# Kernel optimization log

Measured on AMD Instinct MI355X. Metric: run time of the kernel, lower is better.

## Reference

```python
import jax, jax.numpy as jnp
import numpy as np

NY, NU, NH = 64, 64, 256  # Nhidden=256 -> 128 complex eigen pairs
T, NB = 4096, 32          # horizon, batch


def setup_inputs() -> dict:
    key = jax.random.key(0)
    ks = jax.random.split(key, 9)
    return {
        "y0": jax.random.normal(ks[0], (NB, NY), jnp.float32),
        "U": jax.random.normal(ks[1], (T, NB, NU), jnp.float32),
        "lmbd_cont_real": jax.random.uniform(ks[2], (NH // 2,), jnp.float32),
        "lmbd_cont_imag": jax.random.uniform(ks[3], (NH // 2,), jnp.float32),
        "B": jax.random.normal(ks[4], (NH, NU), jnp.float32) / np.sqrt(NU),
        "W_y2x": jax.random.normal(ks[5], (NH, NY), jnp.float32) / np.sqrt(NY),
        "b_y2x": jax.random.normal(ks[6], (NH,), jnp.float32) * 0.01,
        "W_x2y": jax.random.normal(ks[7], (NY, NH), jnp.float32) / np.sqrt(NH),
        "b_x2y": jax.random.normal(ks[8], (NY,), jnp.float32) * 0.01,
    }


def reference(y0, U, lmbd_cont_real, lmbd_cont_imag, B, W_y2x, b_y2x, W_x2y, b_x2y):
    # where A is the real 2x2-block form of complex eigenvalues
    # lambda = r * exp(i*theta), r = exp(-|re|), theta = (pi/2)*im.
    # Original builds A^n explicitly (O(T^2)); an O(T) scan computes the same math.
    H = B.shape[0] // 2
    Bu = jnp.einsum('tbu,hu->tbh', U, B)          # (T, NB, NH)
    r = jnp.exp(-jnp.abs(lmbd_cont_real))
    theta = (jnp.pi / 2) * lmbd_cont_imag
    lr = r * jnp.cos(theta)                        # Re(lambda), (H,)
    li = r * jnp.sin(theta)                        # Im(lambda), (H,)
    x0 = y0 @ W_y2x.T + b_y2x                      # (NB, NH)
    zr0, zi0 = x0[:, :H], x0[:, H:]
    a, b = Bu[:, :, :H], Bu[:, :, H:]

    def step(carry, inp):
        zr, zi = carry
        ak, bk = inp
        nzr = lr * zr - li * zi + ak
        nzi = li * zr + lr * zi + bk
        return (nzr, nzi), (nzr, nzi)

    _, (Xr, Xi) = jax.lax.scan(step, (zr0, zi0), (a, b))
    X = jnp.concatenate([Xr, Xi], axis=-1)         # (T, NB, NH)
    Y = X @ W_x2y.T + b_x2y                        # (T, NB, NY)
    return Y
```

## Files before the change

### kernel.cpp

```cpp
#include <hip/hip_runtime.h>
#include <math.h>

#define TT   4096
#define NBB  32
#define NUU  64
#define NHH  256
#define HH   128
#define NYY  64
#define LCH  8
#define CCH  512
#define SEGN 16
#define CPS  32

#define PI_HALF 1.5707963267948966f

typedef float  f32x16 __attribute__((ext_vector_type(16)));
typedef __bf16 bf16x8 __attribute__((ext_vector_type(8)));
typedef __bf16 bf16x2 __attribute__((ext_vector_type(2)));
typedef unsigned int uint4v __attribute__((ext_vector_type(4)));

__device__ inline int crow(int r, int lane) { return (r & 3) + 8 * (r >> 2) + 4 * (lane >> 5); }
__device__ inline bf16x8 ldfrag(const unsigned short* p) {
    return __builtin_bit_cast(bf16x8, *(const uint4v*)p);
}

__global__ __launch_bounds__(256) void k_prep(
    const float* __restrict__ B, const float* __restrict__ W,
    const float* __restrict__ y0, const float* __restrict__ Wy2x,
    const float* __restrict__ by2x,
    unsigned short* __restrict__ Bp, unsigned short* __restrict__ Wp,
    float2* __restrict__ x0p)
{
    int bx = blockIdx.x, tid = threadIdx.x;
    if (bx < 32) {
        if (tid < HH) {
            int b = bx, ch = tid;
            float xr = by2x[ch], xi = by2x[ch + HH];
            for (int y = 0; y < NYY; ++y) {
                float v = y0[b * NYY + y];
                xr += v * Wy2x[ch * NYY + y];
                xi += v * Wy2x[(ch + HH) * NYY + y];
            }
            x0p[b * HH + ch] = make_float2(xr, xi);
        }
    } else {
        int i = (bx - 32) * 256 + tid;
        Bp[i] = __builtin_bit_cast(unsigned short, (__bf16)B[i]);
        int y = i >> 8, kidx = i & 255;
        Wp[i] = __builtin_bit_cast(unsigned short, (__bf16)W[y * NHH + (kidx & 1) * HH + (kidx >> 1)]);
    }
}

__global__ __launch_bounds__(256, 2) void k_pass1(
    const float* __restrict__ U, const unsigned short* __restrict__ Bp,
    const float* __restrict__ lre, const float* __restrict__ lim,
    float2* __restrict__ E)
{
    __shared__ __align__(16) unsigned short sU[64 * 72];

    const int tid = threadIdx.x, w = tid >> 6, lane = tid & 63;
    const int l31 = lane & 31, kh = lane >> 5;
    const int c = blockIdx.x;
    const int ch = w * 32 + l31;

    float rr = expf(-fabsf(lre[ch])), th = PI_HALF * lim[ch];
    float lr = rr * cosf(th), li = rr * sinf(th);

    bf16x8 bf[2][4];
#pragma unroll
    for (int nt = 0; nt < 2; ++nt)
#pragma unroll
        for (int kk = 0; kk < 4; ++kk)
            bf[nt][kk] = ldfrag(&Bp[(size_t)(nt * HH + ch) * NUU + kk * 16 + kh * 8]);

    float zr[16], zi[16];
#pragma unroll
    for (int r = 0; r < 16; ++r) { zr[r] = 0.f; zi[r] = 0.f; }

    for (int sub = 0; sub < 4; ++sub) {
        {
            int row = tid >> 2, us = (tid & 3) * 16;
            int t = c * LCH + sub * 2 + (row >> 5), b = row & 31;
            const float4* s = (const float4*)(U + ((size_t)t * NBB + b) * NUU + us);
            float4 f0 = s[0], f1 = s[1], f2 = s[2], f3 = s[3];
            bf16x8 p0, p1;
            p0[0]=(__bf16)f0.x; p0[1]=(__bf16)f0.y; p0[2]=(__bf16)f0.z; p0[3]=(__bf16)f0.w;
            p0[4]=(__bf16)f1.x; p0[5]=(__bf16)f1.y; p0[6]=(__bf16)f1.z; p0[7]=(__bf16)f1.w;
            p1[0]=(__bf16)f2.x; p1[1]=(__bf16)f2.y; p1[2]=(__bf16)f2.z; p1[3]=(__bf16)f2.w;
            p1[4]=(__bf16)f3.x; p1[5]=(__bf16)f3.y; p1[6]=(__bf16)f3.z; p1[7]=(__bf16)f3.w;
            *(bf16x8*)&sU[row * 72 + us]     = p0;
            *(bf16x8*)&sU[row * 72 + us + 8] = p1;
        }
        __syncthreads();

        f32x16 acc[2][2];
#pragma unroll
        for (int mt = 0; mt < 2; ++mt)
#pragma unroll
            for (int nt = 0; nt < 2; ++nt)
#pragma unroll
                for (int r = 0; r < 16; ++r) acc[mt][nt][r] = 0.f;

#pragma unroll
        for (int kk = 0; kk < 4; ++kk) {
            bf16x8 a0 = ldfrag(&sU[(l31)      * 72 + kk * 16 + kh * 8]);
            bf16x8 a1 = ldfrag(&sU[(32 + l31) * 72 + kk * 16 + kh * 8]);
            acc[0][0] = __builtin_amdgcn_mfma_f32_32x32x16_bf16(a0, bf[0][kk], acc[0][0], 0, 0, 0);
            acc[0][1] = __builtin_amdgcn_mfma_f32_32x32x16_bf16(a0, bf[1][kk], acc[0][1], 0, 0, 0);
            acc[1][0] = __builtin_amdgcn_mfma_f32_32x32x16_bf16(a1, bf[0][kk], acc[1][0], 0, 0, 0);
            acc[1][1] = __builtin_amdgcn_mfma_f32_32x32x16_bf16(a1, bf[1][kk], acc[1][1], 0, 0, 0);
        }

#pragma unroll
        for (int mt = 0; mt < 2; ++mt)
#pragma unroll
            for (int r = 0; r < 16; ++r) {
                float t0 = fmaf(lr, zr[r], acc[mt][0][r]); t0 = fmaf(-li, zi[r], t0);
                float t1 = fmaf(li, zr[r], acc[mt][1][r]); t1 = fmaf(lr, zi[r], t1);
                zr[r] = t0; zi[r] = t1;
            }
        __syncthreads();
    }

#pragma unroll
    for (int r = 0; r < 16; ++r)
        E[(size_t)c * 4096 + crow(r, lane) * HH + ch] = make_float2(zr[r], zi[r]);
}

__global__ __launch_bounds__(256) void k_cseg(
    const float* __restrict__ lre, const float* __restrict__ lim,
    const float2* __restrict__ E, float2* __restrict__ Esup)
{
    int g = blockIdx.x * 256 + threadIdx.x;
    int chain = g & 4095, seg = g >> 12, ch = chain & 127;
    float rr = expf(-fabsf(lre[ch])), th = PI_HALF * lim[ch];
    float pr = rr * cosf(th), pi = rr * sinf(th);
#pragma unroll
    for (int s = 0; s < 3; ++s) { float nr = pr*pr - pi*pi, ni = 2.f*pr*pi; pr = nr; pi = ni; }
    float sr = 0.f, si = 0.f;
#pragma unroll 8
    for (int j = 0; j < CPS; ++j) {
        float2 e = E[((size_t)seg * CPS + j) * 4096 + chain];
        float nr = pr * sr - pi * si + e.x;
        float ni = pi * sr + pr * si + e.y;
        sr = nr; si = ni;
    }
    Esup[(size_t)seg * 4096 + chain] = make_float2(sr, si);
}

__global__ __launch_bounds__(256) void k_csup(
    const float* __restrict__ lre, const float* __restrict__ lim,
    const float2* __restrict__ x0p, const float2* __restrict__ Esup,
    float2* __restrict__ CarrySup)
{
    int chain = blockIdx.x * 256 + threadIdx.x;
    int ch = chain & 127;
    float rr = expf(-fabsf(lre[ch])), th = PI_HALF * lim[ch];
    float pr = rr * cosf(th), pi = rr * sinf(th);
#pragma unroll
    for (int s = 0; s < 8; ++s) { float nr = pr*pr - pi*pi, ni = 2.f*pr*pi; pr = nr; pi = ni; }
    float2 c0 = x0p[chain];
    float cr = c0.x, ci = c0.y;
#pragma unroll
    for (int s = 0; s < SEGN; ++s) {
        CarrySup[(size_t)s * 4096 + chain] = make_float2(cr, ci);
        float2 e = Esup[(size_t)s * 4096 + chain];
        float nr = pr * cr - pi * ci + e.x;
        float ni = pi * cr + pr * ci + e.y;
        cr = nr; ci = ni;
    }
}

__global__ __launch_bounds__(256) void k_cexp(
    const float* __restrict__ lre, const float* __restrict__ lim,
    const float2* __restrict__ E, const float2* __restrict__ CarrySup,
    float2* __restrict__ Carry)
{
    int g = blockIdx.x * 256 + threadIdx.x;
    int chain = g & 4095, seg = g >> 12, ch = chain & 127;
    float rr = expf(-fabsf(lre[ch])), th = PI_HALF * lim[ch];
    float pr = rr * cosf(th), pi = rr * sinf(th);
#pragma unroll
    for (int s = 0; s < 3; ++s) { float nr = pr*pr - pi*pi, ni = 2.f*pr*pi; pr = nr; pi = ni; }
    float2 cc = CarrySup[(size_t)seg * 4096 + chain];
    float cr = cc.x, ci = cc.y;
#pragma unroll 8
    for (int j = 0; j < CPS; ++j) {
        size_t idx = ((size_t)seg * CPS + j) * 4096 + chain;
        Carry[idx] = make_float2(cr, ci);
        float2 e = E[idx];
        float nr = pr * cr - pi * ci + e.x;
        float ni = pi * cr + pr * ci + e.y;
        cr = nr; ci = ni;
    }
}

__global__ __launch_bounds__(256, 2) void k_pass2(
    const float* __restrict__ U, const unsigned short* __restrict__ Bp,
    const unsigned short* __restrict__ Wp,
    const float* __restrict__ lre, const float* __restrict__ lim,
    const float* __restrict__ bx2y,
    const float2* __restrict__ Carry, float* __restrict__ Y)
{
    __shared__ __align__(16) unsigned short sU[64 * 72];
    __shared__ __align__(16) unsigned short sX[64 * 264];

    const int tid = threadIdx.x, w = tid >> 6, lane = tid & 63;
    const int l31 = lane & 31, kh = lane >> 5;
    const int c = blockIdx.x;
    const int ch = w * 32 + l31;
    const int mtile = w & 1, ntile = w >> 1;

    float rr = expf(-fabsf(lre[ch])), th = PI_HALF * lim[ch];
    float lr = rr * cosf(th), li = rr * sinf(th);
    float ybias = bx2y[ntile * 32 + l31];

    bf16x8 bf[2][4];
#pragma unroll
    for (int nt = 0; nt < 2; ++nt)
#pragma unroll
        for (int kk = 0; kk < 4; ++kk)
            bf[nt][kk] = ldfrag(&Bp[(size_t)(nt * HH + ch) * NUU + kk * 16 + kh * 8]);

    float zr[16], zi[16];
#pragma unroll
    for (int r = 0; r < 16; ++r) {
        float2 v = Carry[(size_t)c * 4096 + crow(r, lane) * HH + ch];
        zr[r] = v.x; zi[r] = v.y;
    }

    for (int sub = 0; sub < 4; ++sub) {
        {
            int row = tid >> 2, us = (tid & 3) * 16;
            int t = c * LCH + sub * 2 + (row >> 5), b = row & 31;
            const float4* s = (const float4*)(U + ((size_t)t * NBB + b) * NUU + us);
            float4 f0 = s[0], f1 = s[1], f2 = s[2], f3 = s[3];
            bf16x8 p0, p1;
            p0[0]=(__bf16)f0.x; p0[1]=(__bf16)f0.y; p0[2]=(__bf16)f0.z; p0[3]=(__bf16)f0.w;
            p0[4]=(__bf16)f1.x; p0[5]=(__bf16)f1.y; p0[6]=(__bf16)f1.z; p0[7]=(__bf16)f1.w;
            p1[0]=(__bf16)f2.x; p1[1]=(__bf16)f2.y; p1[2]=(__bf16)f2.z; p1[3]=(__bf16)f2.w;
            p1[4]=(__bf16)f3.x; p1[5]=(__bf16)f3.y; p1[6]=(__bf16)f3.z; p1[7]=(__bf16)f3.w;
            *(bf16x8*)&sU[row * 72 + us]     = p0;
            *(bf16x8*)&sU[row * 72 + us + 8] = p1;
        }

        if (sub > 0) {
            f32x16 ya;
#pragma unroll
            for (int r = 0; r < 16; ++r) ya[r] = 0.f;
#pragma unroll
            for (int kk = 0; kk < 16; ++kk) {
                bf16x8 xa = ldfrag(&sX[(mtile * 32 + l31) * 264 + kk * 16 + kh * 8]);
                bf16x8 wb = ldfrag(&Wp[(size_t)(ntile * 32 + l31) * NHH + kk * 16 + kh * 8]);
                ya = __builtin_amdgcn_mfma_f32_32x32x16_bf16(xa, wb, ya, 0, 0, 0);
            }
            int t = c * LCH + (sub - 1) * 2 + mtile;
#pragma unroll
            for (int r = 0; r < 16; ++r)
                Y[((size_t)t * NBB + crow(r, lane)) * NYY + ntile * 32 + l31] = ya[r] + ybias;
        }
        __syncthreads();

        f32x16 acc[2][2];
#pragma unroll
        for (int mt = 0; mt < 2; ++mt)
#pragma unroll
            for (int nt = 0; nt < 2; ++nt)
#pragma unroll
                for (int r = 0; r < 16; ++r) acc[mt][nt][r] = 0.f;

#pragma unroll
        for (int kk = 0; kk < 4; ++kk) {
            bf16x8 a0 = ldfrag(&sU[(l31)      * 72 + kk * 16 + kh * 8]);
            bf16x8 a1 = ldfrag(&sU[(32 + l31) * 72 + kk * 16 + kh * 8]);
            acc[0][0] = __builtin_amdgcn_mfma_f32_32x32x16_bf16(a0, bf[0][kk], acc[0][0], 0, 0, 0);
            acc[0][1] = __builtin_amdgcn_mfma_f32_32x32x16_bf16(a0, bf[1][kk], acc[0][1], 0, 0, 0);
            acc[1][0] = __builtin_amdgcn_mfma_f32_32x32x16_bf16(a1, bf[0][kk], acc[1][0], 0, 0, 0);
            acc[1][1] = __builtin_amdgcn_mfma_f32_32x32x16_bf16(a1, bf[1][kk], acc[1][1], 0, 0, 0);
        }

#pragma unroll
        for (int mt = 0; mt < 2; ++mt)
#pragma unroll
            for (int r = 0; r < 16; ++r) {
                float t0 = fmaf(lr, zr[r], acc[mt][0][r]); t0 = fmaf(-li, zi[r], t0);
                float t1 = fmaf(li, zr[r], acc[mt][1][r]); t1 = fmaf(lr, zi[r], t1);
                zr[r] = t0; zi[r] = t1;
                bf16x2 pv; pv[0] = (__bf16)t0; pv[1] = (__bf16)t1;
                *(bf16x2*)&sX[(mt * 32 + crow(r, lane)) * 264 + w * 64 + 2 * l31] = pv;
            }
        __syncthreads();
    }

    {
        f32x16 ya;
#pragma unroll
        for (int r = 0; r < 16; ++r) ya[r] = 0.f;
#pragma unroll
        for (int kk = 0; kk < 16; ++kk) {
            bf16x8 xa = ldfrag(&sX[(mtile * 32 + l31) * 264 + kk * 16 + kh * 8]);
            bf16x8 wb = ldfrag(&Wp[(size_t)(ntile * 32 + l31) * NHH + kk * 16 + kh * 8]);
            ya = __builtin_amdgcn_mfma_f32_32x32x16_bf16(xa, wb, ya, 0, 0, 0);
        }
        int t = c * LCH + 3 * 2 + mtile;
#pragma unroll
        for (int r = 0; r < 16; ++r)
            Y[((size_t)t * NBB + crow(r, lane)) * NYY + ntile * 32 + l31] = ya[r] + ybias;
    }
}

extern "C" void kernel_launch(void* const* d_in, const int* in_sizes, int n_in,
                              void* d_out, int out_size, void* d_ws, size_t ws_size,
                              hipStream_t stream) {
    const float* y0    = (const float*)d_in[0];
    const float* U     = (const float*)d_in[1];
    const float* lre   = (const float*)d_in[2];
    const float* lim   = (const float*)d_in[3];
    const float* B     = (const float*)d_in[4];
    const float* W_y2x = (const float*)d_in[5];
    const float* b_y2x = (const float*)d_in[6];
    const float* W_x2y = (const float*)d_in[7];
    const float* b_x2y = (const float*)d_in[8];
    float* Y = (float*)d_out;

    char* p = (char*)d_ws;
    float2* E        = (float2*)p; p += (size_t)CCH * 4096 * sizeof(float2);
    float2* Carry    = (float2*)p; p += (size_t)CCH * 4096 * sizeof(float2);
    float2* Esup     = (float2*)p; p += (size_t)SEGN * 4096 * sizeof(float2);
    float2* CarrySup = (float2*)p; p += (size_t)SEGN * 4096 * sizeof(float2);
    float2* x0p      = (float2*)p; p += (size_t)4096 * sizeof(float2);
    unsigned short* Bp = (unsigned short*)p; p += 16384 * sizeof(unsigned short);
    unsigned short* Wp = (unsigned short*)p; p += 16384 * sizeof(unsigned short);

    k_prep <<<dim3(96),  dim3(256), 0, stream>>>(B, W_x2y, y0, W_y2x, b_y2x, Bp, Wp, x0p);
    k_pass1<<<dim3(CCH), dim3(256), 0, stream>>>(U, Bp, lre, lim, E);
    k_cseg <<<dim3(256), dim3(256), 0, stream>>>(lre, lim, E, Esup);
    k_csup <<<dim3(16),  dim3(256), 0, stream>>>(lre, lim, x0p, Esup, CarrySup);
    k_cexp <<<dim3(256), dim3(256), 0, stream>>>(lre, lim, E, CarrySup, Carry);
    k_pass2<<<dim3(CCH), dim3(256), 0, stream>>>(U, Bp, Wp, lre, lim, b_x2y, Carry, Y);
}
```

Before: 142.7 us.

## Double-buffer U tiles, pre-swizzle B/W fragments, keep W in registers

k_pass1 and k_pass2 now double-buffer the U staging in shared memory. Each iteration loads the next U slice from global memory into registers before the MFMA work and stores it to the other buffer afterwards, which hides global load latency and removes one barrier per iteration. k_prep writes B and W_x2y in a lane-swizzled fragment order so each lane loads its fragments contiguously. pass2 keeps all 16 W fragments in registers and splits the output GEMM into two accumulator chains. The extra registers and doubled shared memory may cut occupancy under launch_bounds(256,2).

```diff
diff --git a/kernel.cpp b/kernel.cpp
--- a/kernel.cpp
+++ b/kernel.cpp
@@ -23,12 +23,21 @@
 __device__ inline bf16x8 ldfrag(const unsigned short* p) {
     return __builtin_bit_cast(bf16x8, *(const uint4v*)p);
 }
+__device__ inline void store_cvt(unsigned short* dst, float4 f0, float4 f1, float4 f2, float4 f3) {
+    bf16x8 p0, p1;
+    p0[0]=(__bf16)f0.x; p0[1]=(__bf16)f0.y; p0[2]=(__bf16)f0.z; p0[3]=(__bf16)f0.w;
+    p0[4]=(__bf16)f1.x; p0[5]=(__bf16)f1.y; p0[6]=(__bf16)f1.z; p0[7]=(__bf16)f1.w;
+    p1[0]=(__bf16)f2.x; p1[1]=(__bf16)f2.y; p1[2]=(__bf16)f2.z; p1[3]=(__bf16)f2.w;
+    p1[4]=(__bf16)f3.x; p1[5]=(__bf16)f3.y; p1[6]=(__bf16)f3.z; p1[7]=(__bf16)f3.w;
+    *(bf16x8*)dst       = p0;
+    *(bf16x8*)(dst + 8) = p1;
+}
 
 __global__ __launch_bounds__(256) void k_prep(
     const float* __restrict__ B, const float* __restrict__ W,
     const float* __restrict__ y0, const float* __restrict__ Wy2x,
     const float* __restrict__ by2x,
-    unsigned short* __restrict__ Bp, unsigned short* __restrict__ Wp,
+    unsigned short* __restrict__ Bsw, unsigned short* __restrict__ Wsw,
     float2* __restrict__ x0p)
 {
     int bx = blockIdx.x, tid = threadIdx.x;
@@ -45,53 +54,60 @@
         }
     } else {
         int i = (bx - 32) * 256 + tid;
-        Bp[i] = __builtin_bit_cast(unsigned short, (__bf16)B[i]);
-        int y = i >> 8, kidx = i & 255;
-        Wp[i] = __builtin_bit_cast(unsigned short, (__bf16)W[y * NHH + (kidx & 1) * HH + (kidx >> 1)]);
+        {
+            int e = i & 7, lane = (i >> 3) & 63, kk = (i >> 9) & 3, nt = (i >> 11) & 1, w = i >> 12;
+            int l31 = lane & 31, kh = lane >> 5;
+            Bsw[i] = __builtin_bit_cast(unsigned short,
+                     (__bf16)B[(nt * HH + w * 32 + l31) * NUU + kk * 16 + kh * 8 + e]);
+        }
+        {
+            int e = i & 7, lane = (i >> 3) & 63, kk = (i >> 9) & 15, ntl = i >> 13;
+            int l31 = lane & 31, kh = lane >> 5;
+            int kperm = kk * 16 + kh * 8 + e;
+            Wsw[i] = __builtin_bit_cast(unsigned short,
+                     (__bf16)W[(ntl * 32 + l31) * NHH + (kperm & 1) * HH + (kperm >> 1)]);
+        }
     }
 }
 
 __global__ __launch_bounds__(256, 2) void k_pass1(
-    const float* __restrict__ U, const unsigned short* __restrict__ Bp,
+    const float* __restrict__ U, const unsigned short* __restrict__ Bsw,
     const float* __restrict__ lre, const float* __restrict__ lim,
     float2* __restrict__ E)
 {
-    __shared__ __align__(16) unsigned short sU[64 * 72];
+    __shared__ __align__(16) unsigned short sU[2][64 * 72];
 
     const int tid = threadIdx.x, w = tid >> 6, lane = tid & 63;
     const int l31 = lane & 31, kh = lane >> 5;
     const int c = blockIdx.x;
     const int ch = w * 32 + l31;
+    const int srow = tid >> 2, sus = (tid & 3) * 16;
+    const int sb = srow & 31, st_off = srow >> 5;
+
+    bf16x8 bf[2][4];
+#pragma unroll
+    for (int nt = 0; nt < 2; ++nt)
+#pragma unroll
+        for (int kk = 0; kk < 4; ++kk)
+            bf[nt][kk] = ldfrag(&Bsw[((((w * 2 + nt) * 4 + kk) * 64) + lane) * 8]);
 
     float rr = expf(-fabsf(lre[ch])), th = PI_HALF * lim[ch];
     float lr = rr * cosf(th), li = rr * sinf(th);
 
-    bf16x8 bf[2][4];
-#pragma unroll
-    for (int nt = 0; nt < 2; ++nt)
-#pragma unroll
-        for (int kk = 0; kk < 4; ++kk)
-            bf[nt][kk] = ldfrag(&Bp[(size_t)(nt * HH + ch) * NUU + kk * 16 + kh * 8]);
-
+    {
+        const float4* s = (const float4*)(U + ((size_t)(c * LCH + st_off) * NBB + sb) * NUU + sus);
+        store_cvt(&sU[0][srow * 72 + sus], s[0], s[1], s[2], s[3]);
+    }
     float zr[16], zi[16];
 #pragma unroll
     for (int r = 0; r < 16; ++r) { zr[r] = 0.f; zi[r] = 0.f; }
+    __syncthreads();
 
     for (int sub = 0; sub < 4; ++sub) {
-        {
-            int row = tid >> 2, us = (tid & 3) * 16;
-            int t = c * LCH + sub * 2 + (row >> 5), b = row & 31;
-            const float4* s = (const float4*)(U + ((size_t)t * NBB + b) * NUU + us);
-            float4 f0 = s[0], f1 = s[1], f2 = s[2], f3 = s[3];
-            bf16x8 p0, p1;
-            p0[0]=(__bf16)f0.x; p0[1]=(__bf16)f0.y; p0[2]=(__bf16)f0.z; p0[3]=(__bf16)f0.w;
-            p0[4]=(__bf16)f1.x; p0[5]=(__bf16)f1.y; p0[6]=(__bf16)f1.z; p0[7]=(__bf16)f1.w;
-            p1[0]=(__bf16)f2.x; p1[1]=(__bf16)f2.y; p1[2]=(__bf16)f2.z; p1[3]=(__bf16)f2.w;
-            p1[4]=(__bf16)f3.x; p1[5]=(__bf16)f3.y; p1[6]=(__bf16)f3.z; p1[7]=(__bf16)f3.w;
-            *(bf16x8*)&sU[row * 72 + us]     = p0;
-            *(bf16x8*)&sU[row * 72 + us + 8] = p1;
-        }
-        __syncthreads();
+        const int cur = sub & 1;
+        int tld = c * LCH + ((sub < 3) ? (sub + 1) * 2 : 0) + st_off;
+        const float4* s = (const float4*)(U + ((size_t)tld * NBB + sb) * NUU + sus);
+        float4 f0 = s[0], f1 = s[1], f2 = s[2], f3 = s[3];
 
         f32x16 acc[2][2];
 #pragma unroll
@@ -100,17 +116,15 @@
             for (int nt = 0; nt < 2; ++nt)
 #pragma unroll
                 for (int r = 0; r < 16; ++r) acc[mt][nt][r] = 0.f;
-
 #pragma unroll
         for (int kk = 0; kk < 4; ++kk) {
-            bf16x8 a0 = ldfrag(&sU[(l31)      * 72 + kk * 16 + kh * 8]);
-            bf16x8 a1 = ldfrag(&sU[(32 + l31) * 72 + kk * 16 + kh * 8]);
+            bf16x8 a0 = ldfrag(&sU[cur][(l31)      * 72 + kk * 16 + kh * 8]);
+            bf16x8 a1 = ldfrag(&sU[cur][(32 + l31) * 72 + kk * 16 + kh * 8]);
             acc[0][0] = __builtin_amdgcn_mfma_f32_32x32x16_bf16(a0, bf[0][kk], acc[0][0], 0, 0, 0);
             acc[0][1] = __builtin_amdgcn_mfma_f32_32x32x16_bf16(a0, bf[1][kk], acc[0][1], 0, 0, 0);
             acc[1][0] = __builtin_amdgcn_mfma_f32_32x32x16_bf16(a1, bf[0][kk], acc[1][0], 0, 0, 0);
             acc[1][1] = __builtin_amdgcn_mfma_f32_32x32x16_bf16(a1, bf[1][kk], acc[1][1], 0, 0, 0);
         }
-
 #pragma unroll
         for (int mt = 0; mt < 2; ++mt)
 #pragma unroll
@@ -119,6 +133,7 @@
                 float t1 = fmaf(li, zr[r], acc[mt][1][r]); t1 = fmaf(lr, zi[r], t1);
                 zr[r] = t0; zi[r] = t1;
             }
+        store_cvt(&sU[cur ^ 1][srow * 72 + sus], f0, f1, f2, f3);
         __syncthreads();
     }
 
@@ -196,13 +211,13 @@
 }
 
 __global__ __launch_bounds__(256, 2) void k_pass2(
-    const float* __restrict__ U, const unsigned short* __restrict__ Bp,
-    const unsigned short* __restrict__ Wp,
+    const float* __restrict__ U, const unsigned short* __restrict__ Bsw,
+    const unsigned short* __restrict__ Wsw,
     const float* __restrict__ lre, const float* __restrict__ lim,
     const float* __restrict__ bx2y,
     const float2* __restrict__ Carry, float* __restrict__ Y)
 {
-    __shared__ __align__(16) unsigned short sU[64 * 72];
+    __shared__ __align__(16) unsigned short sU[2][64 * 72];
     __shared__ __align__(16) unsigned short sX[64 * 264];
 
     const int tid = threadIdx.x, w = tid >> 6, lane = tid & 63;
@@ -210,17 +225,8 @@
     const int c = blockIdx.x;
     const int ch = w * 32 + l31;
     const int mtile = w & 1, ntile = w >> 1;
-
-    float rr = expf(-fabsf(lre[ch])), th = PI_HALF * lim[ch];
-    float lr = rr * cosf(th), li = rr * sinf(th);
-    float ybias = bx2y[ntile * 32 + l31];
-
-    bf16x8 bf[2][4];
-#pragma unroll
-    for (int nt = 0; nt < 2; ++nt)
-#pragma unroll
-        for (int kk = 0; kk < 4; ++kk)
-            bf[nt][kk] = ldfrag(&Bp[(size_t)(nt * HH + ch) * NUU + kk * 16 + kh * 8]);
+    const int srow = tid >> 2, sus = (tid & 3) * 16;
+    const int sb = srow & 31, st_off = srow >> 5;
 
     float zr[16], zi[16];
 #pragma unroll
@@ -229,37 +235,32 @@
         zr[r] = v.x; zi[r] = v.y;
     }
 
+    bf16x8 bf[2][4];
+#pragma unroll
+    for (int nt = 0; nt < 2; ++nt)
+#pragma unroll
+        for (int kk = 0; kk < 4; ++kk)
+            bf[nt][kk] = ldfrag(&Bsw[((((w * 2 + nt) * 4 + kk) * 64) + lane) * 8]);
+    bf16x8 wf[16];
+#pragma unroll
+    for (int kk = 0; kk < 16; ++kk)
+        wf[kk] = ldfrag(&Wsw[(((ntile * 16 + kk) * 64) + lane) * 8]);
+
+    float rr = expf(-fabsf(lre[ch])), th = PI_HALF * lim[ch];
+    float lr = rr * cosf(th), li = rr * sinf(th);
+    float ybias = bx2y[ntile * 32 + l31];
+
+    {
+        const float4* s = (const float4*)(U + ((size_t)(c * LCH + st_off) * NBB + sb) * NUU + sus);
+        store_cvt(&sU[0][srow * 72 + sus], s[0], s[1], s[2], s[3]);
+    }
+    __syncthreads();
+
     for (int sub = 0; sub < 4; ++sub) {
-        {
-            int row = tid >> 2, us = (tid & 3) * 16;
-            int t = c * LCH + sub * 2 + (row >> 5), b = row & 31;
-            const float4* s = (const float4*)(U + ((size_t)t * NBB + b) * NUU + us);
-            float4 f0 = s[0], f1 = s[1], f2 = s[2], f3 = s[3];
-            bf16x8 p0, p1;
-            p0[0]=(__bf16)f0.x; p0[1]=(__bf16)f0.y; p0[2]=(__bf16)f0.z; p0[3]=(__bf16)f0.w;
-            p0[4]=(__bf16)f1.x; p0[5]=(__bf16)f1.y; p0[6]=(__bf16)f1.z; p0[7]=(__bf16)f1.w;
-            p1[0]=(__bf16)f2.x; p1[1]=(__bf16)f2.y; p1[2]=(__bf16)f2.z; p1[3]=(__bf16)f2.w;
-            p1[4]=(__bf16)f3.x; p1[5]=(__bf16)f3.y; p1[6]=(__bf16)f3.z; p1[7]=(__bf16)f3.w;
-            *(bf16x8*)&sU[row * 72 + us]     = p0;
-            *(bf16x8*)&sU[row * 72 + us + 8] = p1;
-        }
-
-        if (sub > 0) {
-            f32x16 ya;
-#pragma unroll
-            for (int r = 0; r < 16; ++r) ya[r] = 0.f;
-#pragma unroll
-            for (int kk = 0; kk < 16; ++kk) {
-                bf16x8 xa = ldfrag(&sX[(mtile * 32 + l31) * 264 + kk * 16 + kh * 8]);
-                bf16x8 wb = ldfrag(&Wp[(size_t)(ntile * 32 + l31) * NHH + kk * 16 + kh * 8]);
-                ya = __builtin_amdgcn_mfma_f32_32x32x16_bf16(xa, wb, ya, 0, 0, 0);
-            }
-            int t = c * LCH + (sub - 1) * 2 + mtile;
-#pragma unroll
-            for (int r = 0; r < 16; ++r)
-                Y[((size_t)t * NBB + crow(r, lane)) * NYY + ntile * 32 + l31] = ya[r] + ybias;
-        }
-        __syncthreads();
+        const int cur = sub & 1;
+        int tld = c * LCH + ((sub < 3) ? (sub + 1) * 2 : 0) + st_off;
+        const float4* s = (const float4*)(U + ((size_t)tld * NBB + sb) * NUU + sus);
+        float4 f0 = s[0], f1 = s[1], f2 = s[2], f3 = s[3];
 
         f32x16 acc[2][2];
 #pragma unroll
@@ -268,11 +269,10 @@
             for (int nt = 0; nt < 2; ++nt)
 #pragma unroll
                 for (int r = 0; r < 16; ++r) acc[mt][nt][r] = 0.f;
-
 #pragma unroll
         for (int kk = 0; kk < 4; ++kk) {
-            bf16x8 a0 = ldfrag(&sU[(l31)      * 72 + kk * 16 + kh * 8]);
-            bf16x8 a1 = ldfrag(&sU[(32 + l31) * 72 + kk * 16 + kh * 8]);
+            bf16x8 a0 = ldfrag(&sU[cur][(l31)      * 72 + kk * 16 + kh * 8]);
+            bf16x8 a1 = ldfrag(&sU[cur][(32 + l31) * 72 + kk * 16 + kh * 8]);
             acc[0][0] = __builtin_amdgcn_mfma_f32_32x32x16_bf16(a0, bf[0][kk], acc[0][0], 0, 0, 0);
             acc[0][1] = __builtin_amdgcn_mfma_f32_32x32x16_bf16(a0, bf[1][kk], acc[0][1], 0, 0, 0);
             acc[1][0] = __builtin_amdgcn_mfma_f32_32x32x16_bf16(a1, bf[0][kk], acc[1][0], 0, 0, 0);
@@ -290,22 +290,24 @@
                 *(bf16x2*)&sX[(mt * 32 + crow(r, lane)) * 264 + w * 64 + 2 * l31] = pv;
             }
         __syncthreads();
-    }
-
-    {
-        f32x16 ya;
-#pragma unroll
-        for (int r = 0; r < 16; ++r) ya[r] = 0.f;
-#pragma unroll
-        for (int kk = 0; kk < 16; ++kk) {
-            bf16x8 xa = ldfrag(&sX[(mtile * 32 + l31) * 264 + kk * 16 + kh * 8]);
-            bf16x8 wb = ldfrag(&Wp[(size_t)(ntile * 32 + l31) * NHH + kk * 16 + kh * 8]);
-            ya = __builtin_amdgcn_mfma_f32_32x32x16_bf16(xa, wb, ya, 0, 0, 0);
-        }
-        int t = c * LCH + 3 * 2 + mtile;
+
+        f32x16 ya0, ya1;
+#pragma unroll
+        for (int r = 0; r < 16; ++r) { ya0[r] = 0.f; ya1[r] = 0.f; }
+#pragma unroll
+        for (int kk = 0; kk < 16; kk += 2) {
+            bf16x8 xa0 = ldfrag(&sX[(mtile * 32 + l31) * 264 + kk * 16 + kh * 8]);
+            bf16x8 xa1 = ldfrag(&sX[(mtile * 32 + l31) * 264 + (kk + 1) * 16 + kh * 8]);
+            ya0 = __builtin_amdgcn_mfma_f32_32x32x16_bf16(xa0, wf[kk],     ya0, 0, 0, 0);
+            ya1 = __builtin_amdgcn_mfma_f32_32x32x16_bf16(xa1, wf[kk + 1], ya1, 0, 0, 0);
+        }
+        int t = c * LCH + sub * 2 + mtile;
 #pragma unroll
         for (int r = 0; r < 16; ++r)
-            Y[((size_t)t * NBB + crow(r, lane)) * NYY + ntile * 32 + l31] = ya[r] + ybias;
+            Y[((size_t)t * NBB + crow(r, lane)) * NYY + ntile * 32 + l31] = ya0[r] + ya1[r] + ybias;
+
+        store_cvt(&sU[cur ^ 1][srow * 72 + sus], f0, f1, f2, f3);
+        __syncthreads();
     }
 }
 
@@ -329,13 +331,13 @@
     float2* Esup     = (float2*)p; p += (size_t)SEGN * 4096 * sizeof(float2);
     float2* CarrySup = (float2*)p; p += (size_t)SEGN * 4096 * sizeof(float2);
     float2* x0p      = (float2*)p; p += (size_t)4096 * sizeof(float2);
-    unsigned short* Bp = (unsigned short*)p; p += 16384 * sizeof(unsigned short);
-    unsigned short* Wp = (unsigned short*)p; p += 16384 * sizeof(unsigned short);
-
-    k_prep <<<dim3(96),  dim3(256), 0, stream>>>(B, W_x2y, y0, W_y2x, b_y2x, Bp, Wp, x0p);
-    k_pass1<<<dim3(CCH), dim3(256), 0, stream>>>(U, Bp, lre, lim, E);
+    unsigned short* Bsw = (unsigned short*)p; p += 16384 * sizeof(unsigned short);
+    unsigned short* Wsw = (unsigned short*)p; p += 16384 * sizeof(unsigned short);
+
+    k_prep <<<dim3(96),  dim3(256), 0, stream>>>(B, W_x2y, y0, W_y2x, b_y2x, Bsw, Wsw, x0p);
+    k_pass1<<<dim3(CCH), dim3(256), 0, stream>>>(U, Bsw, lre, lim, E);
     k_cseg <<<dim3(256), dim3(256), 0, stream>>>(lre, lim, E, Esup);
     k_csup <<<dim3(16),  dim3(256), 0, stream>>>(lre, lim, x0p, Esup, CarrySup);
     k_cexp <<<dim3(256), dim3(256), 0, stream>>>(lre, lim, E, CarrySup, Carry);
-    k_pass2<<<dim3(CCH), dim3(256), 0, stream>>>(U, Bp, Wp, lre, lim, b_x2y, Carry, Y);
-}
+    k_pass2<<<dim3(CCH), dim3(256), 0, stream>>>(U, Bsw, Wsw, lre, lim, b_x2y, Carry, Y);
+}
```

Measured after the change: 150.7 us. 1.06x slower.
